# Optimization experiments

Measured on AMD Instinct MI355X. Metric: run time of the kernel, lower is better.

## Reference

```python
import jax, jax.numpy as jnp
import numpy as np

THRESHOLD = 0.6


def _conv(x, w, b, pad):
    # x: [B,C,H,W], w: [O,I,kh,kw]
    y = jax.lax.conv_general_dilated(
        x, w, window_strides=(1, 1), padding=[(pad, pad), (pad, pad)],
        dimension_numbers=("NCHW", "OIHW", "NCHW"))
    return y + b[None, :, None, None]


def _avg_pool3(x):
    # F.avg_pool2d(x, 3, stride=1, padding=1) with count_include_pad=True -> divide by 9
    s = jax.lax.reduce_window(x, 0.0, jax.lax.add, (1, 1, 3, 3), (1, 1, 1, 1),
                              [(0, 0), (0, 0), (1, 1), (1, 1)])
    return s / 9.0


def _head(feat, w1, b1, w2, b2, w3, b3):
    h = jax.nn.relu(_conv(feat, w1, b1, 1))
    h = jax.nn.relu(_conv(h, w2, b2, 1))
    return _conv(h, w3, b3, 0)


def _normalize_atten(a):
    # per-sample min-max over spatial dims
    B = a.shape[0]
    flat = a.reshape(B, -1)
    mn = flat.min(axis=1, keepdims=True)
    mx = flat.max(axis=1, keepdims=True)
    return ((flat - mn) / (mx - mn)).reshape(a.shape)


def setup_inputs() -> dict:
    key = jax.random.key(0)
    ks = jax.random.split(key, 16)
    B, C, H, W = 32, 512, 28, 28
    NC = 200
    x = jax.random.normal(ks[0], (B, C, H, W), dtype=jnp.float32)
    label = jax.random.randint(ks[1], (B, NC), 0, 2, dtype=jnp.int32)

    def conv_w(k, o, i, kh):
        std = 1.0 / np.sqrt(i * kh * kh)
        return jax.random.normal(k, (o, i, kh, kh), dtype=jnp.float32) * std

    inp = {"x": x, "label": label}
    # cls head
    inp["w1"] = conv_w(ks[2], 1024, 512, 3); inp["b1"] = jnp.zeros((1024,), jnp.float32)
    inp["w2"] = conv_w(ks[3], 1024, 1024, 3); inp["b2"] = jnp.zeros((1024,), jnp.float32)
    inp["w3"] = conv_w(ks[4], NC, 1024, 1); inp["b3"] = jnp.zeros((NC,), jnp.float32)
    # cls_erase head
    inp["we1"] = conv_w(ks[5], 1024, 512, 3); inp["be1"] = jnp.zeros((1024,), jnp.float32)
    inp["we2"] = conv_w(ks[6], 1024, 1024, 3); inp["be2"] = jnp.zeros((1024,), jnp.float32)
    inp["we3"] = conv_w(ks[7], NC, 1024, 1); inp["be3"] = jnp.zeros((NC,), jnp.float32)
    return inp


def reference(x, label, w1, b1, w2, b2, w3, b3, we1, be1, we2, be2, we3, be3):
    feat = _avg_pool3(x)                              # [B,512,H,W]
    out = _head(feat, w1, b1, w2, b2, w3, b3)         # [B,NC,H,W]
    logits_1 = out.mean(axis=(2, 3))                  # [B,NC]

    # get_atten_map (train mode): average of class maps for positive labels, vectorized
    lab = label.astype(out.dtype)                     # [B,NC] 0/1
    cnt = lab.sum(axis=1)                             # [B]
    atten = jnp.einsum("bc,bchw->bhw", lab, out) / jnp.maximum(cnt, 1.0)[:, None, None]
    atten = _normalize_atten(atten)                   # [B,H,W]

    # erase_feature_maps: zero where atten >= threshold
    mask = jnp.where(atten >= THRESHOLD, 0.0, 1.0)[:, None]  # [B,1,H,W]
    feat_erase = feat * mask

    out_erase = _head(feat_erase, we1, be1, we2, be2, we3, be3)
    logits_ers = out_erase.mean(axis=(2, 3))
    return jax.nn.sigmoid(logits_1), jax.nn.sigmoid(logits_ers)
```

## Files before the change

kernel.cpp:

```cpp
#include <hip/hip_runtime.h>
#include <hip/hip_bf16.h>
#include <stdint.h>


typedef __attribute__((ext_vector_type(8))) short short8;
typedef __attribute__((ext_vector_type(4))) float floatx4;

__device__ __forceinline__ unsigned short f2bf(float f) {
  union { float f; uint32_t u; } cv; cv.f = f;
  uint32_t u = cv.u;
  u += 0x7fffu + ((u >> 16) & 1u);
  return (unsigned short)(u >> 16);
}

__global__ void wprep3(const float* __restrict__ w, unsigned short* __restrict__ wt,
                       int O, int C) {
  int i = blockIdx.x * 256 + threadIdx.x;
  int total = 9 * O * C;
  if (i >= total) return;
  int p = i / (O * C);
  int r = i - p * O * C;
  int o = r / C;
  int c = r - o * C;
  wt[i] = f2bf(w[(size_t)(o * C + c) * 9 + p]);
}

__global__ void wprep1(const float* __restrict__ w, unsigned short* __restrict__ wt,
                       int O, int OP, int C) {
  int i = blockIdx.x * 256 + threadIdx.x;
  if (i >= OP * C) return;
  int o = i / C, c = i - o * C;
  wt[i] = (o < O) ? f2bf(w[(size_t)o * C + c]) : (unsigned short)0;
}

__global__ void avgpool_k(const float* __restrict__ x, unsigned short* __restrict__ fp) {
  const int C = 512;
  int b = blockIdx.x, r = blockIdx.y, cg = blockIdx.z;
  int t = threadIdx.x;
  __shared__ float xs[3 * 128 * 29];
  if (r == 0 || r == 29) {
    for (int i = t; i < 32 * 128; i += 256) {
      int c = i & 127, col = i >> 7;
      fp[((size_t)(b * 30 + r) * 32 + col) * C + cg * 128 + c] = 0;
    }
    return;
  }
  for (int i = t; i < 3 * 128 * 28; i += 256) {
    int dy = i / 3584;
    int rem = i - dy * 3584;
    int c = rem / 28, fx = rem - c * 28;
    int fy = r - 2 + dy;
    float v = (fy >= 0 && fy < 28)
                  ? x[((size_t)(b * 512 + cg * 128 + c) * 28 + fy) * 28 + fx]
                  : 0.f;
    xs[(dy * 128 + c) * 29 + fx] = v;
  }
  __syncthreads();
  for (int i = t; i < 32 * 128; i += 256) {
    int c = i & 127, col = i >> 7;
    float v = 0.f;
    if (col >= 1 && col <= 28) {
      int fx0 = col - 1;
#pragma unroll
      for (int dy = 0; dy < 3; ++dy)
#pragma unroll
        for (int dx = 0; dx < 3; ++dx) {
          int fx = fx0 - 1 + dx;
          if (fx >= 0 && fx < 28) v += xs[(dy * 128 + c) * 29 + fx];
        }
      v *= (1.f / 9.f);
    }
    fp[((size_t)(b * 30 + r) * 32 + col) * C + cg * 128 + c] = f2bf(v);
  }
}

__global__ void zero_borders(unsigned short* __restrict__ h1,
                             unsigned short* __restrict__ h2, int Mch) {
  int i = blockIdx.x * 256 + threadIdx.x;
  int vch = Mch >> 3;
  int perbuf = 32 * 176 * vch;
  if (i >= 2 * perbuf) return;
  unsigned short* h = (i < perbuf) ? h1 : h2;
  int j = (i < perbuf) ? i : i - perbuf;
  int cv = j % vch;
  int rr = j / vch;
  int bidx = rr / 176, e = rr - bidx * 176;
  int row, col;
  if (e < 32)      { row = 0;  col = e; }
  else if (e < 64) { row = 29; col = e - 32; }
  else {
    int q = e - 64;
    row = 1 + (q >> 2);
    int k = q & 3;
    col = (k == 0) ? 0 : 28 + k;
  }
  size_t addr = ((size_t)(bidx * 30 + row) * 32 + col) * Mch + cv * 8;
  *(uint4*)&h[addr] = (uint4){0u, 0u, 0u, 0u};
}

template <int P, int RELU, int PADOUT>
__global__ __launch_bounds__(256, 2)
void conv_mfma(const unsigned short* __restrict__ fin,
               const unsigned short* __restrict__ wt,
               const float* __restrict__ bias,
               void* __restrict__ outp, int C, int M, int OB) {
  const int tid = threadIdx.x;
  const int lane = tid & 63;
  const int wave = tid >> 6;
  const int hB = wave & 1;
  const int wo = wave >> 1;
  const int ln = lane & 15;
  const int kq = lane >> 4;

  const int id = blockIdx.x;
  const int xo = id / 112;
  const int s  = id - xo * 112;
  const int yo = s % 7;
  const int bz = s / 7;

  const int o0 = xo * 128 + wo * 64;
  const int wO0 = xo * 128;
  const int yo0 = yo * 4;
  const int b0 = bz * 2;
  const int bb = b0 + hB;

  __shared__ unsigned short ldsA[2 * 1536 * 8];
  __shared__ unsigned short ldsW[4 * 512 * 8];

  int baserc[7];
#pragma unroll
  for (int mi = 0; mi < 7; ++mi) {
    int n = mi * 16 + ln;
    int y = n / 28, x = n - y * 28;
    baserc[mi] = y * 32 + x;
  }
  const int wbase = wo * 2048 + ln * 32 + ((kq ^ (ln & 3)) << 3);

  floatx4 acc[7][4];
#pragma unroll
  for (int mi = 0; mi < 7; ++mi)
#pragma unroll
    for (int ni = 0; ni < 4; ++ni)
      acc[mi][ni] = (floatx4){0.f, 0.f, 0.f, 0.f};

  const size_t fin_base0 = (size_t)(b0 * 30 + yo0) * 32 * C;
  const size_t fin_base1 = (size_t)((b0 + 1) * 30 + yo0) * 32 * C;

  const int rA = tid >> 2;
  const int cgA = (tid & 3) ^ (rA & 3);

  auto stageA = [&](int ck, int buf) {
#pragma unroll
    for (int it = 0; it < 6; ++it) {
      int wb = (it >= 3) ? 1 : 0;
      int it3 = it - wb * 3;
      int rc = it3 * 64 + rA;
      size_t goff = (wb ? fin_base1 : fin_base0) + (size_t)rc * C + ck + cgA * 8;
      unsigned short* lp = &ldsA[(unsigned)(buf * 1536 + wb * 768 + it3 * 256 + wave * 64) << 3];
      __builtin_amdgcn_global_load_lds((const uint32_t*)(fin + goff), (uint32_t*)lp,
                                       16, 0, 0);
    }
  };
  auto stageW = [&](int p, int ck, int q) {
#pragma unroll
    for (int it = 0; it < 2; ++it) {
      int row = it * 64 + rA;
      size_t goff = (size_t)(p * M + wO0 + row) * C + ck + cgA * 8;
      unsigned short* lp = &ldsW[(unsigned)(q * 512 + it * 256 + wave * 64) << 3];
      __builtin_amdgcn_global_load_lds((const uint32_t*)(wt + goff), (uint32_t*)lp,
                                       16, 0, 0);
    }
  };

  stageA(0, 0);
  stageW(0, 0, 0);
  if (P == 9) { stageW(1, 0, 1); stageW(2, 0, 2); }

  int cur = 0;
  int rq0 = 0;
  for (int ck = 0; ck < C; ck += 32) {
    const bool last = (ck + 32 >= C);
#pragma unroll
    for (int p = 0; p < P; ++p) {
      const bool fin_phase = last && (p == P - 1);

      __builtin_amdgcn_s_barrier();
      __builtin_amdgcn_sched_barrier(0);

      if (P == 9) {
        if (!(last && p >= 6))
          stageW(p < 6 ? p + 3 : p - 6, p < 6 ? ck : ck + 32, (rq0 + p + 3) & 3);
      } else {
        if (!last) stageW(0, ck + 32, (rq0 + p + 1) & 3);
      }
      if (p == 0 && !last) stageA(ck + 32, cur ^ 1);

      if (P == 9) {
        if (fin_phase)           asm volatile("s_waitcnt vmcnt(0)" ::: "memory");
        else if (last && p == 6) asm volatile("s_waitcnt vmcnt(4)" ::: "memory");
        else if (last && p == 7) asm volatile("s_waitcnt vmcnt(2)" ::: "memory");
        else if (last)           asm volatile("s_waitcnt vmcnt(6)" ::: "memory");
        else if (p <= 3)         asm volatile("s_waitcnt vmcnt(12)" ::: "memory");
        else                     asm volatile("s_waitcnt vmcnt(6)" ::: "memory");
      } else {
        if (last)                asm volatile("s_waitcnt vmcnt(0)" ::: "memory");
        else                     asm volatile("s_waitcnt vmcnt(8)" ::: "memory");
      }
      __builtin_amdgcn_sched_barrier(0);

      __builtin_amdgcn_s_barrier();
      __builtin_amdgcn_sched_barrier(0);
      asm volatile("" ::: "memory");

      const unsigned short* wrd = &ldsW[(unsigned)(((rq0 + p) & 3) << 12)];
      const unsigned short* ard = &ldsA[cur ? 12288 : 0];
      int dy, dx;
      if (P == 1) { dy = 1; dx = 1; } else { dy = p / 3; dx = p - dy * 3; }
      short8 wf[4];
#pragma unroll
      for (int ni = 0; ni < 4; ++ni)
        wf[ni] = *(const short8*)(const void*)&wrd[wbase + ni * 512];
      short8 af[7];
#pragma unroll
      for (int mi = 0; mi < 7; ++mi) {
        int rc = baserc[mi] + dy * 32 + dx;
        int u = hB * 768 + (rc << 2) + (kq ^ (rc & 3));
        af[mi] = *(const short8*)(const void*)&ard[(unsigned)u << 3];
      }
      __builtin_amdgcn_s_setprio(1);
#pragma unroll
      for (int mi = 0; mi < 7; ++mi)
#pragma unroll
        for (int ni = 0; ni < 4; ++ni)
          acc[mi][ni] = __builtin_amdgcn_mfma_f32_16x16x32_bf16(af[mi], wf[ni],
                                                                acc[mi][ni], 0, 0, 0);
      __builtin_amdgcn_s_setprio(0);
    }
    rq0 = (rq0 + P) & 3;
    cur ^= 1;
  }

  float bia[4];
#pragma unroll
  for (int ni = 0; ni < 4; ++ni) {
    int o = o0 + ni * 16 + ln;
    bia[ni] = (o < OB) ? bias[o] : 0.f;
  }
#pragma unroll
  for (int mi = 0; mi < 7; ++mi) {
#pragma unroll
    for (int j = 0; j < 4; ++j) {
      int n = mi * 16 + kq * 4 + j;
      int y = n / 28, x = n - y * 28;
#pragma unroll
      for (int ni = 0; ni < 4; ++ni) {
        int o = o0 + ni * 16 + ln;
        float v = acc[mi][ni][j] + bia[ni];
        if (RELU) v = fmaxf(v, 0.f);
        if (PADOUT) {
          size_t addr = ((size_t)(bb * 30 + yo0 + y + 1) * 32 + (x + 1)) * M + o;
          ((unsigned short*)outp)[addr] = f2bf(v);
        } else {
          size_t addr = ((size_t)bb * 784 + (yo0 + y) * 28 + x) * M + o;
          ((float*)outp)[addr] = v;
        }
      }
    }
  }
}

template <int DO_ATTEN>
__global__ void logits_atten(const float* __restrict__ ob, const int* __restrict__ label,
                             float* __restrict__ outp, float* __restrict__ mask) {
  int b = blockIdx.x, t = threadIdx.x;
  const float* base = ob + (size_t)b * 784 * 256;
  float s = 0.f;
#pragma unroll 16
  for (int n = 0; n < 784; ++n) s += base[(size_t)n * 256 + t];
  if (t < 200) outp[b * 200 + t] = 1.f / (1.f + expf(-s * (1.f / 784.f)));

  if (DO_ATTEN) {
    __shared__ float labf[256];
    __shared__ float red[16];
    labf[t] = (t < 200) ? (float)label[b * 200 + t] : 0.f;
    __syncthreads();
    float att[4];
    float mn = 1e30f, mx = -1e30f;
#pragma unroll
    for (int i = 0; i < 4; ++i) {
      int n = t + i * 256;
      float a = 0.f;
      if (n < 784) {
        const float* rowp = base + (size_t)n * 256;
#pragma unroll 8
        for (int c = 0; c < 200; ++c) a += labf[c] * rowp[c];
        mn = fminf(mn, a);
        mx = fmaxf(mx, a);
      }
      att[i] = a;
    }
    for (int off = 32; off; off >>= 1) {
      mn = fminf(mn, __shfl_down(mn, off, 64));
      mx = fmaxf(mx, __shfl_down(mx, off, 64));
    }
    if ((t & 63) == 0) { red[(t >> 6) * 2] = mn; red[(t >> 6) * 2 + 1] = mx; }
    __syncthreads();
    if (t == 0) {
      float a = red[0], c = red[1];
      for (int wv = 1; wv < 4; ++wv) {
        a = fminf(a, red[wv * 2]);
        c = fmaxf(c, red[wv * 2 + 1]);
      }
      red[0] = a; red[1] = c;
    }
    __syncthreads();
    float gmn = red[0];
    float inv = 1.f / (red[1] - gmn);
#pragma unroll
    for (int i = 0; i < 4; ++i) {
      int n = t + i * 256;
      if (n < 784)
        mask[b * 784 + n] = ((att[i] - gmn) * inv >= 0.6f) ? 0.f : 1.f;
    }
  }
}

__global__ void erase_k(unsigned short* __restrict__ fp, const float* __restrict__ mask) {
  int i = blockIdx.x * 256 + threadIdx.x;
  if (i >= 32 * 28 * 28 * 512) return;
  int c = i & 511;
  int r2 = i >> 9;
  int xcol = r2 % 28;
  int r3 = r2 / 28;
  int y = r3 % 28;
  int b = r3 / 28;
  if (mask[b * 784 + y * 28 + xcol] == 0.f)
    fp[((size_t)(b * 30 + y + 1) * 32 + (xcol + 1)) * 512 + c] = 0;
}

extern "C" void kernel_launch(void* const* d_in, const int* in_sizes, int n_in,
                              void* d_out, int out_size, void* d_ws, size_t ws_size,
                              hipStream_t stream) {
  const float* x   = (const float*)d_in[0];
  const int* label = (const int*)d_in[1];
  const float* w1  = (const float*)d_in[2];
  const float* b1  = (const float*)d_in[3];
  const float* w2  = (const float*)d_in[4];
  const float* b2  = (const float*)d_in[5];
  const float* w3  = (const float*)d_in[6];
  const float* b3  = (const float*)d_in[7];
  const float* we1 = (const float*)d_in[8];
  const float* be1 = (const float*)d_in[9];
  const float* we2 = (const float*)d_in[10];
  const float* be2 = (const float*)d_in[11];
  const float* we3 = (const float*)d_in[12];
  const float* be3 = (const float*)d_in[13];
  float* outv = (float*)d_out;

  char* wp = (char*)d_ws;
  unsigned short* featp = (unsigned short*)wp; wp += 31457280;
  unsigned short* h1p   = (unsigned short*)wp; wp += 62914560;
  unsigned short* h2p   = (unsigned short*)wp; wp += 62914560;
  unsigned short* Wt1   = (unsigned short*)wp; wp += 9437184;
  unsigned short* Wt2   = (unsigned short*)wp; wp += 18874368;
  unsigned short* Wt3   = (unsigned short*)wp; wp += 524288;
  float* outbuf         = (float*)wp;          wp += 25690112;
  float* maskb          = (float*)wp;          wp += 100352;

  zero_borders<<<5632, 256, 0, stream>>>(h1p, h2p, 1024);
  avgpool_k<<<dim3(32, 30, 4), 256, 0, stream>>>(x, featp);
  wprep3<<<(9 * 1024 * 512 + 255) / 256, 256, 0, stream>>>(w1, Wt1, 1024, 512);
  wprep3<<<(9 * 1024 * 1024 + 255) / 256, 256, 0, stream>>>(w2, Wt2, 1024, 1024);
  wprep1<<<(256 * 1024 + 255) / 256, 256, 0, stream>>>(w3, Wt3, 200, 256, 1024);

  conv_mfma<9, 1, 1><<<896, 256, 0, stream>>>(featp, Wt1, b1, h1p, 512, 1024, 1024);
  conv_mfma<9, 1, 1><<<896, 256, 0, stream>>>(h1p, Wt2, b2, h2p, 1024, 1024, 1024);
  conv_mfma<1, 0, 0><<<224, 256, 0, stream>>>(h2p, Wt3, b3, outbuf, 1024, 256, 200);
  logits_atten<1><<<32, 256, 0, stream>>>(outbuf, label, outv, maskb);

  erase_k<<<(32 * 28 * 28 * 512 + 255) / 256, 256, 0, stream>>>(featp, maskb);
  wprep3<<<(9 * 1024 * 512 + 255) / 256, 256, 0, stream>>>(we1, Wt1, 1024, 512);
  wprep3<<<(9 * 1024 * 1024 + 255) / 256, 256, 0, stream>>>(we2, Wt2, 1024, 1024);
  wprep1<<<(256 * 1024 + 255) / 256, 256, 0, stream>>>(we3, Wt3, 200, 256, 1024);
  conv_mfma<9, 1, 1><<<896, 256, 0, stream>>>(featp, Wt1, be1, h1p, 512, 1024, 1024);
  conv_mfma<9, 1, 1><<<896, 256, 0, stream>>>(h1p, Wt2, be2, h2p, 1024, 1024, 1024);
  conv_mfma<1, 0, 0><<<224, 256, 0, stream>>>(h2p, Wt3, be3, outbuf, 1024, 256, 200);
  logits_atten<0><<<32, 256, 0, stream>>>(outbuf, nullptr, outv + 6400, nullptr);
}
```

Baseline: 3.634 ms.

## Stage conv epilogue through LDS, reorder block mapping, add cache hint on input loads

The padded bf16 conv epilogue now writes results into shared memory and then stores them as 16-byte vectors per output row, replacing scattered 2-byte global stores. The block index mapping now puts the output-channel tile in the low bits, so consecutive blocks share the same input activation tile, which improves L2 reuse. Input global-to-LDS loads get a different cache-policy flag. This adds an extra barrier and an LDS round trip in the epilogue, and the shared LDS buffer is reused for staging.

```diff
diff --git a/kernel.cpp b/kernel.cpp
--- a/kernel.cpp
+++ b/kernel.cpp
@@ -98,7 +98,7 @@
   *(uint4*)&h[addr] = (uint4){0u, 0u, 0u, 0u};
 }
 
-template <int P, int RELU, int PADOUT>
+template <int P, int RELU, int PADOUT, int XBITS>
 __global__ __launch_bounds__(256, 2)
 void conv_mfma(const unsigned short* __restrict__ fin,
                const unsigned short* __restrict__ wt,
@@ -113,8 +113,8 @@
   const int kq = lane >> 4;
 
   const int id = blockIdx.x;
-  const int xo = id / 112;
-  const int s  = id - xo * 112;
+  const int xo = id & ((1 << XBITS) - 1);
+  const int s  = id >> XBITS;
   const int yo = s % 7;
   const int bz = s / 7;
 
@@ -124,8 +124,9 @@
   const int b0 = bz * 2;
   const int bb = b0 + hB;
 
-  __shared__ unsigned short ldsA[2 * 1536 * 8];
-  __shared__ unsigned short ldsW[4 * 512 * 8];
+  __shared__ unsigned short ldsAll[40960];
+  unsigned short* ldsA = ldsAll;
+  unsigned short* ldsW = ldsAll + 24576;
 
   int baserc[7];
 #pragma unroll
@@ -158,7 +159,7 @@
       size_t goff = (wb ? fin_base1 : fin_base0) + (size_t)rc * C + ck + cgA * 8;
       unsigned short* lp = &ldsA[(unsigned)(buf * 1536 + wb * 768 + it3 * 256 + wave * 64) << 3];
       __builtin_amdgcn_global_load_lds((const uint32_t*)(fin + goff), (uint32_t*)lp,
-                                       16, 0, 0);
+                                       16, 0, 2);
     }
   };
   auto stageW = [&](int p, int ck, int q) {
@@ -246,21 +247,46 @@
     int o = o0 + ni * 16 + ln;
     bia[ni] = (o < OB) ? bias[o] : 0.f;
   }
-#pragma unroll
-  for (int mi = 0; mi < 7; ++mi) {
-#pragma unroll
-    for (int j = 0; j < 4; ++j) {
-      int n = mi * 16 + kq * 4 + j;
+
+  if (PADOUT) {
+    __builtin_amdgcn_s_barrier();
+    unsigned short* ep = ldsAll + wave * 8064;
+#pragma unroll
+    for (int mi = 0; mi < 7; ++mi)
+#pragma unroll
+      for (int j = 0; j < 4; ++j) {
+        int n = mi * 16 + kq * 4 + j;
+#pragma unroll
+        for (int ni = 0; ni < 4; ++ni) {
+          float v = acc[mi][ni][j] + bia[ni];
+          if (RELU) v = fmaxf(v, 0.f);
+          ep[n * 72 + ni * 16 + ln] = f2bf(v);
+        }
+      }
+    asm volatile("s_waitcnt lgkmcnt(0)" ::: "memory");
+    __builtin_amdgcn_sched_barrier(0);
+    const int rsub = lane >> 3;
+    const int oseg = (lane & 7) * 8;
+#pragma unroll
+    for (int it = 0; it < 14; ++it) {
+      int n = it * 8 + rsub;
       int y = n / 28, x = n - y * 28;
-#pragma unroll
-      for (int ni = 0; ni < 4; ++ni) {
-        int o = o0 + ni * 16 + ln;
-        float v = acc[mi][ni][j] + bia[ni];
-        if (RELU) v = fmaxf(v, 0.f);
-        if (PADOUT) {
-          size_t addr = ((size_t)(bb * 30 + yo0 + y + 1) * 32 + (x + 1)) * M + o;
-          ((unsigned short*)outp)[addr] = f2bf(v);
-        } else {
+      uint4 v = *(const uint4*)&ep[n * 72 + oseg];
+      size_t addr = ((size_t)(bb * 30 + yo0 + y + 1) * 32 + (x + 1)) * M + o0 + oseg;
+      *(uint4*)&((unsigned short*)outp)[addr] = v;
+    }
+  } else {
+#pragma unroll
+    for (int mi = 0; mi < 7; ++mi) {
+#pragma unroll
+      for (int j = 0; j < 4; ++j) {
+        int n = mi * 16 + kq * 4 + j;
+        int y = n / 28, x = n - y * 28;
+#pragma unroll
+        for (int ni = 0; ni < 4; ++ni) {
+          int o = o0 + ni * 16 + ln;
+          float v = acc[mi][ni][j] + bia[ni];
+          if (RELU) v = fmaxf(v, 0.f);
           size_t addr = ((size_t)bb * 784 + (yo0 + y) * 28 + x) * M + o;
           ((float*)outp)[addr] = v;
         }
@@ -373,17 +399,17 @@
   wprep3<<<(9 * 1024 * 1024 + 255) / 256, 256, 0, stream>>>(w2, Wt2, 1024, 1024);
   wprep1<<<(256 * 1024 + 255) / 256, 256, 0, stream>>>(w3, Wt3, 200, 256, 1024);
 
-  conv_mfma<9, 1, 1><<<896, 256, 0, stream>>>(featp, Wt1, b1, h1p, 512, 1024, 1024);
-  conv_mfma<9, 1, 1><<<896, 256, 0, stream>>>(h1p, Wt2, b2, h2p, 1024, 1024, 1024);
-  conv_mfma<1, 0, 0><<<224, 256, 0, stream>>>(h2p, Wt3, b3, outbuf, 1024, 256, 200);
+  conv_mfma<9, 1, 1, 3><<<896, 256, 0, stream>>>(featp, Wt1, b1, h1p, 512, 1024, 1024);
+  conv_mfma<9, 1, 1, 3><<<896, 256, 0, stream>>>(h1p, Wt2, b2, h2p, 1024, 1024, 1024);
+  conv_mfma<1, 0, 0, 1><<<224, 256, 0, stream>>>(h2p, Wt3, b3, outbuf, 1024, 256, 200);
   logits_atten<1><<<32, 256, 0, stream>>>(outbuf, label, outv, maskb);
 
   erase_k<<<(32 * 28 * 28 * 512 + 255) / 256, 256, 0, stream>>>(featp, maskb);
   wprep3<<<(9 * 1024 * 512 + 255) / 256, 256, 0, stream>>>(we1, Wt1, 1024, 512);
   wprep3<<<(9 * 1024 * 1024 + 255) / 256, 256, 0, stream>>>(we2, Wt2, 1024, 1024);
   wprep1<<<(256 * 1024 + 255) / 256, 256, 0, stream>>>(we3, Wt3, 200, 256, 1024);
-  conv_mfma<9, 1, 1><<<896, 256, 0, stream>>>(featp, Wt1, be1, h1p, 512, 1024, 1024);
-  conv_mfma<9, 1, 1><<<896, 256, 0, stream>>>(h1p, Wt2, be2, h2p, 1024, 1024, 1024);
-  conv_mfma<1, 0, 0><<<224, 256, 0, stream>>>(h2p, Wt3, be3, outbuf, 1024, 256, 200);
+  conv_mfma<9, 1, 1, 3><<<896, 256, 0, stream>>>(featp, Wt1, be1, h1p, 512, 1024, 1024);
+  conv_mfma<9, 1, 1, 3><<<896, 256, 0, stream>>>(h1p, Wt2, be2, h2p, 1024, 1024, 1024);
+  conv_mfma<1, 0, 0, 1><<<224, 256, 0, stream>>>(h2p, Wt3, be3, outbuf, 1024, 256, 200);
   logits_atten<0><<<32, 256, 0, stream>>>(outbuf, nullptr, outv + 6400, nullptr);
 }
```

After: 3.387 ms. 1.07x faster.
